# Optimization experiments

Hardware: AMD Instinct MI355X
Metric: run time of the kernel (lower is better)

## Reference

```python
import jax, jax.numpy as jnp
import numpy as np

N = 200_000          # active voxels
CIN, COUT = 64, 128  # in_filters, out_filters
GRID = (32, 480, 480)  # sparse spatial shape (D, H, W)
NEG_SLOPE = 0.01     # nn.LeakyReLU default
EPS = 1e-5           # BatchNorm1d default


def _build_nbrs():
    """Build rulebook-style neighbor tables for the two submanifold kernels.

    Returns nbr31 [9, N] for kernel (3,1,3) and nbr13 [9, N] for kernel (1,3,3).
    Entry == N means 'no active neighbor' (maps to a zero pad row).
    """
    rng = np.random.default_rng(0)
    prod = GRID[0] * GRID[1] * GRID[2]
    lin = rng.choice(prod, size=N, replace=False)
    z, y, x = np.unravel_index(lin, GRID)
    lut = np.full(prod, N, dtype=np.int64)
    lut[lin] = np.arange(N)

    def nbrs(offsets):
        out = np.full((len(offsets), N), N, dtype=np.int32)
        for k, (dz, dy, dx) in enumerate(offsets):
            zz, yy, xx = z + dz, y + dy, x + dx
            valid = ((zz >= 0) & (zz < GRID[0]) & (yy >= 0) & (yy < GRID[1])
                     & (xx >= 0) & (xx < GRID[2]))
            l2 = (zz * GRID[1] + yy) * GRID[2] + xx
            out[k, valid] = lut[l2[valid]].astype(np.int32)
        return out

    off31 = [(dz, 0, dx) for dz in (-1, 0, 1) for dx in (-1, 0, 1)]  # (3,1,3)
    off13 = [(0, dy, dx) for dy in (-1, 0, 1) for dx in (-1, 0, 1)]  # (1,3,3)
    return nbrs(off31), nbrs(off13)


def setup_inputs() -> dict:
    key = jax.random.key(0)
    ks = jax.random.split(key, 5)
    nbr31, nbr13 = _build_nbrs()
    s_in = (2.0 / (9 * CIN)) ** 0.5
    s_out = (2.0 / (9 * COUT)) ** 0.5
    ones = jnp.ones((COUT,), jnp.float32)
    zeros = jnp.zeros((COUT,), jnp.float32)
    return {
        "feats": jax.random.normal(ks[0], (N, CIN), jnp.float32),
        "W1": jax.random.normal(ks[1], (9, CIN, COUT), jnp.float32) * s_in,
        "W1_2": jax.random.normal(ks[2], (9, COUT, COUT), jnp.float32) * s_out,
        "W2": jax.random.normal(ks[3], (9, CIN, COUT), jnp.float32) * s_in,
        "W3": jax.random.normal(ks[4], (9, COUT, COUT), jnp.float32) * s_out,
        "g0": ones, "b0": zeros,      # bn0  (init: weight=1, bias=0)
        "g0_2": ones, "b0_2": zeros,  # bn0_2
        "g1": ones, "b1": zeros,      # bn1
        "g2": ones, "b2": zeros,      # bn2
        "nbr31": jnp.asarray(nbr31),
        "nbr13": jnp.asarray(nbr13),
    }


def _subm_conv(f, W, nbr):
    # f [N, Cin], W [9, Cin, Cout], nbr [9, N] -> [N, Cout]
    fp = jnp.concatenate([f, jnp.zeros((1, f.shape[1]), f.dtype)], axis=0)
    g = fp[nbr]  # gather: [9, N, Cin]
    return jnp.einsum("knc,kcd->nd", g, W)


def _lrelu(f):
    return jnp.where(f >= 0, f, NEG_SLOPE * f)


def _bn(f, gamma, beta):
    # BatchNorm1d training-mode batch stats (biased variance) over voxel dim
    m = jnp.mean(f, axis=0)
    v = jnp.mean(jnp.square(f), axis=0) - m * m
    return (f - m) * jax.lax.rsqrt(v + EPS) * gamma + beta


def reference(feats, W1, W1_2, W2, W3, g0, b0, g0_2, b0_2, g1, b1, g2, b2,
              nbr31, nbr13):
    shortcut = _bn(_lrelu(_subm_conv(feats, W1, nbr31)), g0, b0)
    shortcut = _bn(_lrelu(_subm_conv(shortcut, W1_2, nbr13)), g0_2, b0_2)
    resA = _bn(_lrelu(_subm_conv(feats, W2, nbr13)), g1, b1)
    resA = _bn(_lrelu(_subm_conv(resA, W3, nbr31)), g2, b2)
    return resA + shortcut
```

## Files before the change

### kernel.cpp

```cpp
#include <hip/hip_runtime.h>

#define NV 200000
#define NCH 391
#define PCAP 56
#define CG 3125
#define PN 3516
#define RB1 110

typedef __attribute__((ext_vector_type(8))) short sh8;
typedef __attribute__((ext_vector_type(4))) float f32x4;
typedef __attribute__((ext_vector_type(2))) unsigned int u32x2;

__device__ inline unsigned short f2bf(float f) {
  unsigned int u = __builtin_bit_cast(unsigned int, f);
  u += 0x7FFFu + ((u >> 16) & 1u);
  return (unsigned short)(u >> 16);
}
__device__ inline float bf2f(unsigned short h) {
  unsigned int u = ((unsigned int)h) << 16;
  return __builtin_bit_cast(float, u);
}
__device__ inline float lrelu(float v) { return v >= 0.f ? v : 0.01f * v; }

__global__ __launch_bounds__(256) void prep_k(
    const float* __restrict__ W1, const float* __restrict__ W12,
    const float* __restrict__ W2, const float* __restrict__ W3,
    unsigned short* __restrict__ T1, unsigned short* __restrict__ T12,
    unsigned short* __restrict__ T2, unsigned short* __restrict__ T3,
    const int* __restrict__ nbr31, const int* __restrict__ nbr13,
    int2* __restrict__ pairs, int* __restrict__ cc) {
  __shared__ unsigned short lt[64 * 130];
  __shared__ int base_s[4];
  __shared__ int run;
  int bx = blockIdx.x;
  const int tid = threadIdx.x;
  if (bx < 36) {
    const float* src;
    unsigned short* dst;
    int cin, k;
    if (bx < 9) { src = W1; dst = T1; cin = 64; k = bx; }
    else if (bx < 18) { src = W2; dst = T2; cin = 64; k = bx - 9; }
    else if (bx < 27) { src = W12; dst = T12; cin = 128; k = bx - 18; }
    else { src = W3; dst = T3; cin = 128; k = bx - 27; }
    src += (size_t)k * cin * 128;
    dst += (size_t)k * 128 * cin;
    const int cmask = cin - 1;
    const int csh = (cin == 64) ? 6 : 7;
    for (int h = 0; h < 2; ++h) {
      if (h) __syncthreads();
      const int tot = cin * 64;
      for (int e = tid; e < tot; e += 256) {
        const int c = e >> 6, dd = e & 63;
        lt[dd * 130 + c] = f2bf(src[c * 128 + h * 64 + dd]);
      }
      __syncthreads();
      for (int o = tid; o < tot; o += 256) {
        const int dl = o >> csh, c = o & cmask;
        dst[(size_t)(h * 64 + dl) * cin + c] = lt[dl * 130 + c];
      }
    }
    return;
  }
  bx -= 36;
  const int slot = bx / NCH, chunk = bx % NCH;
  const int table = slot >> 3, kk = slot & 7;
  const int k = kk + (kk >= 4);
  const int* nb = (table ? nbr13 : nbr31) + (size_t)k * NV;
  const int lane = tid & 63, wv = tid >> 6;
  if (tid == 0) run = 0;
  __syncthreads();
  int2* pw = pairs + (size_t)(slot * NCH + chunk) * PCAP;
#pragma unroll
  for (int i = 0; i < 2; ++i) {
    const int n = chunk * 512 + i * 256 + tid;
    const int val = (n < NV) ? nb[n] : NV;
    const bool valid = (val != NV);
    const unsigned long long m = __ballot(valid);
    const int loff = __popcll(m & ((1ull << lane) - 1ull));
    if (lane == 0) base_s[wv] = __popcll(m);
    __syncthreads();
    int wbase = run;
    for (int w = 0; w < wv; ++w) wbase += base_s[w];
    if (valid) {
      const int pos = wbase + loff;
      if (pos < PCAP) {
        int2 pr;
        pr.x = val;
        pr.y = n;
        pw[pos] = pr;
      }
    }
    __syncthreads();
    if (tid == 0) run += base_s[0] + base_s[1] + base_s[2] + base_s[3];
    __syncthreads();
  }
  if (tid == 0) cc[slot * NCH + chunk] = min(run, PCAP);
}

#define STATS_EMIT(ACC, PART, PROW)                                             \
  {                                                                             \
    f32x4 ssum[2], ssq[2];                                                      \
    _Pragma("unroll") for (int mt = 0; mt < 2; ++mt) {                          \
      ssum[mt] = (f32x4){0.f, 0.f, 0.f, 0.f};                                   \
      ssq[mt] = (f32x4){0.f, 0.f, 0.f, 0.f};                                    \
      _Pragma("unroll") for (int nt = 0; nt < 4; ++nt)                          \
          _Pragma("unroll") for (int q = 0; q < 4; ++q) {                       \
        const float f = lrelu(ACC[mt][nt][q]);                                  \
        ssum[mt][q] += f;                                                       \
        ssq[mt][q] += f * f;                                                    \
      }                                                                         \
      _Pragma("unroll") for (int off = 1; off < 16; off <<= 1)                  \
          _Pragma("unroll") for (int q = 0; q < 4; ++q) {                       \
        ssum[mt][q] += __shfl_xor(ssum[mt][q], off);                            \
        ssq[mt][q] += __shfl_xor(ssq[mt][q], off);                              \
      }                                                                         \
      if (l15 == 0) {                                                           \
        const int d0 = (wv * 2 + mt) * 16 + l4 * 4;                             \
        *(f32x4*)(PART + (size_t)(PROW)*256 + d0) = ssum[mt];                   \
        *(f32x4*)(PART + (size_t)(PROW)*256 + 128 + d0) = ssq[mt];              \
      }                                                                         \
    }                                                                           \
  }

#define TILE_OUT(ACC, YPTR)                                                     \
  {                                                                             \
    __syncthreads();                                                            \
    _Pragma("unroll") for (int mt = 0; mt < 2; ++mt)                            \
        _Pragma("unroll") for (int nt = 0; nt < 4; ++nt) {                      \
      u32x2 pk;                                                                 \
      pk[0] = (unsigned)f2bf(ACC[mt][nt][0]) |                                  \
              ((unsigned)f2bf(ACC[mt][nt][1]) << 16);                           \
      pk[1] = (unsigned)f2bf(ACC[mt][nt][2]) |                                  \
              ((unsigned)f2bf(ACC[mt][nt][3]) << 16);                           \
      *(u32x2*)(&lds[(nt * 16 + l15) * 136 + (wv * 2 + mt) * 16 + l4 * 4]) = pk;\
    }                                                                           \
    __syncthreads();                                                            \
    _Pragma("unroll") for (int j = 0; j < 4; ++j) {                             \
      const int row = j * 16 + (tid >> 4);                                      \
      const int c16 = tid & 15;                                                 \
      const sh8 v = *(const sh8*)(&lds[row * 136 + c16 * 8]);                   \
      *(sh8*)(YPTR + (size_t)(row0 + row) * 128 + c16 * 8) = v;                 \
    }                                                                           \
  }

__global__ __launch_bounds__(256) void center2_k(
    const float* __restrict__ X, const unsigned short* __restrict__ W1t,
    const unsigned short* __restrict__ W2t, unsigned short* __restrict__ Y1,
    unsigned short* __restrict__ Y2, float* __restrict__ PA,
    float* __restrict__ PB) {
  constexpr int CIN = 64, CH = 8;
  __shared__ unsigned short lds[64 * 136];
  const int tid = threadIdx.x, lane = tid & 63, wv = tid >> 6;
  const int l15 = lane & 15, l4 = lane >> 4;
  const int prow = blockIdx.x;
  const int row0 = prow * 64;
  const int js = tid & 7;
#pragma unroll
  for (int i = 0; i < 2; ++i) {
    const int r = (i * 256 + tid) >> 3;
    const f32x4 a = *(const f32x4*)(X + (size_t)(row0 + r) * CIN + js * 8);
    const f32x4 b = *(const f32x4*)(X + (size_t)(row0 + r) * CIN + js * 8 + 4);
    sh8 o;
#pragma unroll
    for (int j = 0; j < 4; ++j) {
      o[j] = (short)f2bf(a[j]);
      o[4 + j] = (short)f2bf(b[j]);
    }
    *(sh8*)(lds + ((size_t)r * CH + (js ^ (r & 7))) * 8) = o;
  }
  __syncthreads();

  f32x4 acc1[2][4], acc2[2][4];
#pragma unroll
  for (int mt = 0; mt < 2; ++mt)
#pragma unroll
    for (int nt = 0; nt < 4; ++nt) {
      acc1[mt][nt] = (f32x4){0.f, 0.f, 0.f, 0.f};
      acc2[mt][nt] = (f32x4){0.f, 0.f, 0.f, 0.f};
    }
  const unsigned short* W1K = W1t + (size_t)(4 * 128) * CIN;
  const unsigned short* W2K = W2t + (size_t)(4 * 128) * CIN;
#pragma unroll
  for (int s = 0; s < 2; ++s) {
    sh8 aw1[2], aw2[2];
#pragma unroll
    for (int mt = 0; mt < 2; ++mt) {
      const int d = (wv * 2 + mt) * 16 + l15;
      aw1[mt] = *(const sh8*)(W1K + (size_t)d * CIN + s * 32 + l4 * 8);
      aw2[mt] = *(const sh8*)(W2K + (size_t)d * CIN + s * 32 + l4 * 8);
    }
#pragma unroll
    for (int nt = 0; nt < 4; ++nt) {
      const int r = nt * 16 + l15;
      const int j = s * 4 + l4;
      const sh8 bx = *(const sh8*)(lds + ((size_t)r * CH + (j ^ (r & 7))) * 8);
#pragma unroll
      for (int mt = 0; mt < 2; ++mt) {
        acc1[mt][nt] =
            __builtin_amdgcn_mfma_f32_16x16x32_bf16(aw1[mt], bx, acc1[mt][nt], 0, 0, 0);
        acc2[mt][nt] =
            __builtin_amdgcn_mfma_f32_16x16x32_bf16(aw2[mt], bx, acc2[mt][nt], 0, 0, 0);
      }
    }
  }
  STATS_EMIT(acc1, PA, prow)
  STATS_EMIT(acc2, PB, prow)
  TILE_OUT(acc1, Y1)
  __syncthreads();
  TILE_OUT(acc2, Y2)
}

__global__ __launch_bounds__(256) void c128m_k(
    const unsigned short* __restrict__ y1, const unsigned short* __restrict__ y2,
    const unsigned short* __restrict__ T12, const unsigned short* __restrict__ T3,
    const float* __restrict__ ab, unsigned short* __restrict__ ysc,
    unsigned short* __restrict__ y3, float* __restrict__ PA,
    float* __restrict__ PB) {
  constexpr int CIN = 128, CH = 16;
  __shared__ unsigned short lds[64 * 136];
  const int bx = blockIdx.x;
  const bool first = bx < CG;
  const unsigned short* X = first ? y1 : y2;
  const unsigned short* Wt = first ? T12 : T3;
  const float* abp = first ? ab : ab + 256;
  unsigned short* Y = first ? ysc : y3;
  float* PART = first ? PA : PB;
  const int prow = first ? bx : bx - CG;
  const int row0 = prow * 64;
  const int tid = threadIdx.x, lane = tid & 63, wv = tid >> 6;
  const int l15 = lane & 15, l4 = lane >> 4;
  const int js = tid & 15;
  const f32x4 aL = *(const f32x4*)(abp + js * 8);
  const f32x4 aH = *(const f32x4*)(abp + js * 8 + 4);
  const f32x4 bL = *(const f32x4*)(abp + 128 + js * 8);
  const f32x4 bH = *(const f32x4*)(abp + 128 + js * 8 + 4);
#pragma unroll
  for (int i = 0; i < 4; ++i) {
    const int r = (i * 256 + tid) >> 4;
    const sh8 v = *(const sh8*)(X + (size_t)(row0 + r) * CIN + js * 8);
    sh8 o;
#pragma unroll
    for (int j = 0; j < 4; ++j) {
      o[j] = (short)f2bf(lrelu(bf2f((unsigned short)v[j])) * aL[j] + bL[j]);
      o[4 + j] = (short)f2bf(lrelu(bf2f((unsigned short)v[4 + j])) * aH[j] + bH[j]);
    }
    *(sh8*)(lds + ((size_t)r * CH + (js ^ (r & 7))) * 8) = o;
  }
  __syncthreads();

  f32x4 acc[2][4];
#pragma unroll
  for (int mt = 0; mt < 2; ++mt)
#pragma unroll
    for (int nt = 0; nt < 4; ++nt) acc[mt][nt] = (f32x4){0.f, 0.f, 0.f, 0.f};

  const unsigned short* WtK = Wt + (size_t)(4 * 128) * CIN;
#pragma unroll
  for (int s = 0; s < 4; ++s) {
    sh8 aw[2];
#pragma unroll
    for (int mt = 0; mt < 2; ++mt) {
      const int d = (wv * 2 + mt) * 16 + l15;
      aw[mt] = *(const sh8*)(WtK + (size_t)d * CIN + s * 32 + l4 * 8);
    }
#pragma unroll
    for (int nt = 0; nt < 4; ++nt) {
      const int r = nt * 16 + l15;
      const int j = s * 4 + l4;
      const sh8 bxv = *(const sh8*)(lds + ((size_t)r * CH + (j ^ (r & 7))) * 8);
#pragma unroll
      for (int mt = 0; mt < 2; ++mt)
        acc[mt][nt] =
            __builtin_amdgcn_mfma_f32_16x16x32_bf16(aw[mt], bxv, acc[mt][nt], 0, 0, 0);
    }
  }
  STATS_EMIT(acc, PART, prow)
  TILE_OUT(acc, Y)
}

__global__ __launch_bounds__(256) void off64_k(
    const float* __restrict__ X, const unsigned short* __restrict__ T1,
    const unsigned short* __restrict__ T2, const int2* __restrict__ pairs,
    const int* __restrict__ cc, unsigned short* __restrict__ y1,
    unsigned short* __restrict__ y2, float* __restrict__ PA,
    float* __restrict__ PB) {
  constexpr int CIN = 64, CH = 8;
  const int layer = blockIdx.x / NCH, chunk = blockIdx.x % NCH;
  const unsigned short* Wt = layer ? T2 : T1;
  unsigned short* Y = layer ? y2 : y1;
  float* PD = layer ? PB : PA;
  const int* ccl = cc + layer * 8 * NCH;
  const int2* pl = pairs + (size_t)layer * 8 * NCH * PCAP;
  __shared__ unsigned short tile[64 * CIN];
  const int tid = threadIdx.x, lane = tid & 63, wv = tid >> 6;
  const int l15 = lane & 15, l4 = lane >> 4;
  const int js = tid & 7;
  f32x4 ds[2], dq[2];
#pragma unroll
  for (int mt = 0; mt < 2; ++mt) {
    ds[mt] = (f32x4){0.f, 0.f, 0.f, 0.f};
    dq[mt] = (f32x4){0.f, 0.f, 0.f, 0.f};
  }

  for (int kk = 0; kk < 8; ++kk) {
    const int n0 = ccl[kk * NCH + chunk];
    if (n0 == 0) continue;
    const int k = kk + (kk >= 4);
    const unsigned short* WtK = Wt + (size_t)k * 128 * CIN;
    const int2* pw = pl + (size_t)(kk * NCH + chunk) * PCAP;
    __syncthreads();
#pragma unroll
    for (int i = 0; i < 2; ++i) {
      const int r = (i * 256 + tid) >> 3;
      const int in = (r < n0) ? pw[r].x : NV;
      sh8 o = (sh8){0, 0, 0, 0, 0, 0, 0, 0};
      if (in != NV) {
        const f32x4 a = *(const f32x4*)(X + (size_t)in * CIN + js * 8);
        const f32x4 b = *(const f32x4*)(X + (size_t)in * CIN + js * 8 + 4);
#pragma unroll
        for (int j = 0; j < 4; ++j) {
          o[j] = (short)f2bf(a[j]);
          o[4 + j] = (short)f2bf(b[j]);
        }
      }
      *(sh8*)(tile + ((size_t)r * CH + (js ^ (r & 7))) * 8) = o;
    }
    __syncthreads();

    f32x4 acc[2][4];
#pragma unroll
    for (int mt = 0; mt < 2; ++mt)
#pragma unroll
      for (int nt = 0; nt < 4; ++nt) acc[mt][nt] = (f32x4){0.f, 0.f, 0.f, 0.f};
#pragma unroll
    for (int s = 0; s < 2; ++s) {
      sh8 aw[2];
#pragma unroll
      for (int mt = 0; mt < 2; ++mt) {
        const int d = (wv * 2 + mt) * 16 + l15;
        aw[mt] = *(const sh8*)(WtK + (size_t)d * CIN + s * 32 + l4 * 8);
      }
#pragma unroll
      for (int nt = 0; nt < 4; ++nt) {
        const int r = nt * 16 + l15;
        const int j = s * 4 + l4;
        const sh8 bxv = *(const sh8*)(tile + ((size_t)r * CH + (j ^ (r & 7))) * 8);
#pragma unroll
        for (int mt = 0; mt < 2; ++mt)
          acc[mt][nt] =
              __builtin_amdgcn_mfma_f32_16x16x32_bf16(aw[mt], bxv, acc[mt][nt], 0, 0, 0);
      }
    }
#pragma unroll
    for (int mt = 0; mt < 2; ++mt)
#pragma unroll
      for (int nt = 0; nt < 4; ++nt) {
        const int rr = nt * 16 + l15;
        const int out = (rr < n0) ? pw[rr].y : NV;
        if (out == NV) continue;
        const int d0 = (wv * 2 + mt) * 16 + l4 * 4;
        unsigned short* p = Y + (size_t)out * 128 + d0;
        const u32x2 old = *(const u32x2*)p;
        u32x2 nw;
        float of[4], sf[4];
        of[0] = bf2f((unsigned short)(old[0] & 0xffff));
        of[1] = bf2f((unsigned short)(old[0] >> 16));
        of[2] = bf2f((unsigned short)(old[1] & 0xffff));
        of[3] = bf2f((unsigned short)(old[1] >> 16));
#pragma unroll
        for (int q = 0; q < 4; ++q) {
          sf[q] = of[q] + acc[mt][nt][q];
          const float ln = lrelu(sf[q]), lo = lrelu(of[q]);
          ds[mt][q] += ln - lo;
          dq[mt][q] += ln * ln - lo * lo;
        }
        nw[0] = (unsigned)f2bf(sf[0]) | ((unsigned)f2bf(sf[1]) << 16);
        nw[1] = (unsigned)f2bf(sf[2]) | ((unsigned)f2bf(sf[3]) << 16);
        *(u32x2*)p = nw;
      }
  }
#pragma unroll
  for (int mt = 0; mt < 2; ++mt) {
#pragma unroll
    for (int off = 1; off < 16; off <<= 1)
#pragma unroll
      for (int q = 0; q < 4; ++q) {
        ds[mt][q] += __shfl_xor(ds[mt][q], off);
        dq[mt][q] += __shfl_xor(dq[mt][q], off);
      }
    if (l15 == 0) {
      const int d0 = (wv * 2 + mt) * 16 + l4 * 4;
      *(f32x4*)(PD + (size_t)(CG + chunk) * 256 + d0) = ds[mt];
      *(f32x4*)(PD + (size_t)(CG + chunk) * 256 + 128 + d0) = dq[mt];
    }
  }
}

__global__ __launch_bounds__(256) void off128m_k(
    const unsigned short* __restrict__ y1, const unsigned short* __restrict__ y2,
    const unsigned short* __restrict__ T12, const unsigned short* __restrict__ T3,
    const int2* __restrict__ pairs, const int* __restrict__ cc,
    const float* __restrict__ ab, unsigned short* __restrict__ ysc,
    unsigned short* __restrict__ y3, float* __restrict__ PA,
    float* __restrict__ PB) {
  constexpr int CIN = 128, CH = 16;
  const int lay = blockIdx.x / NCH, chunk = blockIdx.x % NCH;
  const unsigned short* X = lay ? y2 : y1;
  const unsigned short* Wt = lay ? T3 : T12;
  const float* abp = lay ? ab + 256 : ab;
  unsigned short* Y = lay ? y3 : ysc;
  float* PD = lay ? PB : PA;
  const int2* pt = pairs + (lay ? 0 : (size_t)8 * NCH * PCAP);
  const int* ct = cc + (lay ? 0 : 8 * NCH);
  __shared__ unsigned short tile[64 * CIN];
  const int tid = threadIdx.x, lane = tid & 63, wv = tid >> 6;
  const int l15 = lane & 15, l4 = lane >> 4;
  const int js = tid & 15;
  const f32x4 aL = *(const f32x4*)(abp + js * 8);
  const f32x4 aH = *(const f32x4*)(abp + js * 8 + 4);
  const f32x4 bL = *(const f32x4*)(abp + 128 + js * 8);
  const f32x4 bH = *(const f32x4*)(abp + 128 + js * 8 + 4);
  f32x4 ds[2], dq[2];
#pragma unroll
  for (int mt = 0; mt < 2; ++mt) {
    ds[mt] = (f32x4){0.f, 0.f, 0.f, 0.f};
    dq[mt] = (f32x4){0.f, 0.f, 0.f, 0.f};
  }

  for (int kk = 0; kk < 8; ++kk) {
    const int n0 = ct[kk * NCH + chunk];
    if (n0 == 0) continue;
    const int k = kk + (kk >= 4);
    const unsigned short* WtK = Wt + (size_t)k * 128 * CIN;
    const int2* pw = pt + (size_t)(kk * NCH + chunk) * PCAP;
    __syncthreads();
#pragma unroll
    for (int i = 0; i < 4; ++i) {
      const int r = (i * 256 + tid) >> 4;
      const int in = (r < n0) ? pw[r].x : NV;
      sh8 o = (sh8){0, 0, 0, 0, 0, 0, 0, 0};
      if (in != NV) {
        const sh8 v = *(const sh8*)(X + (size_t)in * CIN + js * 8);
#pragma unroll
        for (int j = 0; j < 4; ++j) {
          o[j] = (short)f2bf(lrelu(bf2f((unsigned short)v[j])) * aL[j] + bL[j]);
          o[4 + j] = (short)f2bf(lrelu(bf2f((unsigned short)v[4 + j])) * aH[j] + bH[j]);
        }
      }
      *(sh8*)(tile + ((size_t)r * CH + (js ^ (r & 7))) * 8) = o;
    }
    __syncthreads();

    f32x4 acc[2][4];
#pragma unroll
    for (int mt = 0; mt < 2; ++mt)
#pragma unroll
      for (int nt = 0; nt < 4; ++nt) acc[mt][nt] = (f32x4){0.f, 0.f, 0.f, 0.f};
#pragma unroll
    for (int s = 0; s < 4; ++s) {
      sh8 aw[2];
#pragma unroll
      for (int mt = 0; mt < 2; ++mt) {
        const int d = (wv * 2 + mt) * 16 + l15;
        aw[mt] = *(const sh8*)(WtK + (size_t)d * CIN + s * 32 + l4 * 8);
      }
#pragma unroll
      for (int nt = 0; nt < 4; ++nt) {
        const int r = nt * 16 + l15;
        const int j = s * 4 + l4;
        const sh8 bxv = *(const sh8*)(tile + ((size_t)r * CH + (j ^ (r & 7))) * 8);
#pragma unroll
        for (int mt = 0; mt < 2; ++mt)
          acc[mt][nt] =
              __builtin_amdgcn_mfma_f32_16x16x32_bf16(aw[mt], bxv, acc[mt][nt], 0, 0, 0);
      }
    }
#pragma unroll
    for (int mt = 0; mt < 2; ++mt)
#pragma unroll
      for (int nt = 0; nt < 4; ++nt) {
        const int rr = nt * 16 + l15;
        const int out = (rr < n0) ? pw[rr].y : NV;
        if (out == NV) continue;
        const int d0 = (wv * 2 + mt) * 16 + l4 * 4;
        unsigned short* p = Y + (size_t)out * 128 + d0;
        const u32x2 old = *(const u32x2*)p;
        u32x2 nw;
        float of[4], sf[4];
        of[0] = bf2f((unsigned short)(old[0] & 0xffff));
        of[1] = bf2f((unsigned short)(old[0] >> 16));
        of[2] = bf2f((unsigned short)(old[1] & 0xffff));
        of[3] = bf2f((unsigned short)(old[1] >> 16));
#pragma unroll
        for (int q = 0; q < 4; ++q) {
          sf[q] = of[q] + acc[mt][nt][q];
          const float ln = lrelu(sf[q]), lo = lrelu(of[q]);
          ds[mt][q] += ln - lo;
          dq[mt][q] += ln * ln - lo * lo;
        }
        nw[0] = (unsigned)f2bf(sf[0]) | ((unsigned)f2bf(sf[1]) << 16);
        nw[1] = (unsigned)f2bf(sf[2]) | ((unsigned)f2bf(sf[3]) << 16);
        *(u32x2*)p = nw;
      }
  }
#pragma unroll
  for (int mt = 0; mt < 2; ++mt) {
#pragma unroll
    for (int off = 1; off < 16; off <<= 1)
#pragma unroll
      for (int q = 0; q < 4; ++q) {
        ds[mt][q] += __shfl_xor(ds[mt][q], off);
        dq[mt][q] += __shfl_xor(dq[mt][q], off);
      }
    if (l15 == 0) {
      const int d0 = (wv * 2 + mt) * 16 + l4 * 4;
      *(f32x4*)(PD + (size_t)(CG + chunk) * 256 + d0) = ds[mt];
      *(f32x4*)(PD + (size_t)(CG + chunk) * 256 + 128 + d0) = dq[mt];
    }
  }
}

__global__ __launch_bounds__(256) void red1_k(const float* __restrict__ PA,
                                              const float* __restrict__ PB,
                                              float* __restrict__ RA,
                                              float* __restrict__ RB) {
  const int tb = blockIdx.x / RB1;
  const int b = blockIdx.x % RB1;
  const float* P = tb ? PB : PA;
  float* R = tb ? RB : RA;
  const int c = threadIdx.x;
  const int r0 = b * 32;
  const int r1 = (r0 + 32 < PN) ? r0 + 32 : PN;
  float s = 0.f;
#pragma unroll 4
  for (int r = r0; r < r1; ++r) s += P[(size_t)r * 256 + c];
  R[(size_t)b * 256 + c] = s;
}

__global__ __launch_bounds__(1024) void fin2_k(
    const float* __restrict__ RA, const float* __restrict__ gA,
    const float* __restrict__ btA, float* __restrict__ abA,
    const float* __restrict__ RB, const float* __restrict__ gB,
    const float* __restrict__ btB, float* __restrict__ abB) {
  const float* R = blockIdx.x ? RB : RA;
  const float* g = blockIdx.x ? gB : gA;
  const float* bt = blockIdx.x ? btB : btA;
  float* abo = blockIdx.x ? abB : abA;
  __shared__ float S[1024];
  const int t = threadIdx.x;
  const int c = t & 255, grp = t >> 8;
  float s = 0.f;
  for (int b = grp; b < RB1; b += 4) s += R[(size_t)b * 256 + c];
  S[t] = s;
  __syncthreads();
  if (t < 256) S[t] = S[t] + S[256 + t] + S[512 + t] + S[768 + t];
  __syncthreads();
  if (t < 128) {
    const float m = S[t] * (1.0f / (float)NV);
    const float v = S[128 + t] * (1.0f / (float)NV) - m * m;
    const float a = g[t] * rsqrtf(v + 1e-5f);
    abo[t] = a;
    abo[128 + t] = bt[t] - m * a;
  }
}

__global__ __launch_bounds__(256) void final_k(const unsigned short* __restrict__ y3,
                                               const unsigned short* __restrict__ ysc,
                                               const float* __restrict__ ab3,
                                               const float* __restrict__ ab1,
                                               float* __restrict__ out) {
  const long i = (long)blockIdx.x * 256 + threadIdx.x;
  if (i >= (long)NV * 16) return;
  const long base = i * 8;
  const int c0 = (int)(base & 127);
  const sh8 v3 = *(const sh8*)(y3 + base);
  const sh8 vs = *(const sh8*)(ysc + base);
  const f32x4 a3L = *(const f32x4*)(ab3 + c0);
  const f32x4 a3H = *(const f32x4*)(ab3 + c0 + 4);
  const f32x4 b3L = *(const f32x4*)(ab3 + 128 + c0);
  const f32x4 b3H = *(const f32x4*)(ab3 + 128 + c0 + 4);
  const f32x4 a1L = *(const f32x4*)(ab1 + c0);
  const f32x4 a1H = *(const f32x4*)(ab1 + c0 + 4);
  const f32x4 b1L = *(const f32x4*)(ab1 + 128 + c0);
  const f32x4 b1H = *(const f32x4*)(ab1 + 128 + c0 + 4);
  f32x4 oL, oH;
#pragma unroll
  for (int j = 0; j < 4; ++j) {
    oL[j] = a3L[j] * lrelu(bf2f((unsigned short)v3[j])) + b3L[j] +
            a1L[j] * lrelu(bf2f((unsigned short)vs[j])) + b1L[j];
    oH[j] = a3H[j] * lrelu(bf2f((unsigned short)v3[4 + j])) + b3H[j] +
            a1H[j] * lrelu(bf2f((unsigned short)vs[4 + j])) + b1H[j];
  }
  *(f32x4*)(out + base) = oL;
  *(f32x4*)(out + base + 4) = oH;
}

extern "C" void kernel_launch(void* const* d_in, const int* in_sizes, int n_in,
                              void* d_out, int out_size, void* d_ws, size_t ws_size,
                              hipStream_t stream) {
  const float* feats = (const float*)d_in[0];
  const float* W1 = (const float*)d_in[1];
  const float* W12 = (const float*)d_in[2];
  const float* W2 = (const float*)d_in[3];
  const float* W3 = (const float*)d_in[4];
  const float* g0 = (const float*)d_in[5];
  const float* b0 = (const float*)d_in[6];
  const float* g02 = (const float*)d_in[7];
  const float* b02 = (const float*)d_in[8];
  const float* g1 = (const float*)d_in[9];
  const float* b1 = (const float*)d_in[10];
  const float* g2 = (const float*)d_in[11];
  const float* b2 = (const float*)d_in[12];
  const int* nbr31 = (const int*)d_in[13];
  const int* nbr13 = (const int*)d_in[14];
  float* out = (float*)d_out;

  char* ws = (char*)d_ws;
  size_t off = 0;
  auto alloc = [&](size_t bytes) {
    char* p = ws + off;
    off = (off + bytes + 255) & ~(size_t)255;
    return p;
  };

  unsigned short* T1 = (unsigned short*)alloc((size_t)9 * 128 * 64 * 2);
  unsigned short* T2 = (unsigned short*)alloc((size_t)9 * 128 * 64 * 2);
  unsigned short* T12 = (unsigned short*)alloc((size_t)9 * 128 * 128 * 2);
  unsigned short* T3 = (unsigned short*)alloc((size_t)9 * 128 * 128 * 2);
  unsigned short* y1 = (unsigned short*)alloc((size_t)NV * 128 * 2);
  unsigned short* y2 = (unsigned short*)alloc((size_t)NV * 128 * 2);
  unsigned short* ysc = (unsigned short*)alloc((size_t)NV * 128 * 2);
  unsigned short* y3 = (unsigned short*)alloc((size_t)NV * 128 * 2);
  float* PA = (float*)alloc((size_t)PN * 256 * 4);
  float* PB = (float*)alloc((size_t)PN * 256 * 4);
  float* RA = (float*)alloc((size_t)RB1 * 256 * 4);
  float* RB = (float*)alloc((size_t)RB1 * 256 * 4);
  float* ab = (float*)alloc(1024 * 4);
  int* cc = (int*)alloc((size_t)16 * NCH * 4);
  int2* pairs = (int2*)alloc((size_t)16 * NCH * PCAP * 8);


  prep_k<<<36 + 16 * NCH, 256, 0, stream>>>(W1, W12, W2, W3, T1, T12, T2, T3,
                                            nbr31, nbr13, pairs, cc);
  center2_k<<<CG, 256, 0, stream>>>(feats, T1, T2, y1, y2, PA, PB);
  off64_k<<<2 * NCH, 256, 0, stream>>>(feats, T1, T2, pairs, cc, y1, y2, PA, PB);
  red1_k<<<2 * RB1, 256, 0, stream>>>(PA, PB, RA, RB);
  fin2_k<<<2, 1024, 0, stream>>>(RA, g0, b0, ab + 0, RB, g1, b1, ab + 256);
  c128m_k<<<2 * CG, 256, 0, stream>>>(y1, y2, T12, T3, ab, ysc, y3, PA, PB);
  off128m_k<<<2 * NCH, 256, 0, stream>>>(y1, y2, T12, T3, pairs, cc, ab, ysc, y3,
                                         PA, PB);
  red1_k<<<2 * RB1, 256, 0, stream>>>(PA, PB, RA, RB);
  fin2_k<<<2, 1024, 0, stream>>>(RA, g02, b02, ab + 512, RB, g2, b2, ab + 768);
  final_k<<<12500, 256, 0, stream>>>(y3, ysc, ab + 768, ab + 512, out);
}
```

Baseline: 288.0 us.

## Replace compacted pair lists with output-stationary per-tile neighbour gather convolution

Drops the prep-time compaction of neighbour pairs and the separate offset kernels, which did scattered bf16 read-modify-write updates to the outputs. Each 64-row output tile now loops over all nine kernel offsets. For each offset it gathers neighbour rows directly from the nbr tables into LDS and accumulates with MFMA in registers. A block-wide OR skips an offset only when the tile has no valid neighbour at all. This removes kernel launches, the pair buffers and the scatter RMW traffic, but runs much more MFMA work on mostly zero rows and adds a barrier per offset.

```diff
diff --git a/kernel.cpp b/kernel.cpp
--- a/kernel.cpp
+++ b/kernel.cpp
@@ -1,11 +1,9 @@
 #include <hip/hip_runtime.h>
 
 #define NV 200000
-#define NCH 391
-#define PCAP 56
 #define CG 3125
-#define PN 3516
-#define RB1 110
+#define PN 3125
+#define RB1 98
 
 typedef __attribute__((ext_vector_type(8))) short sh8;
 typedef __attribute__((ext_vector_type(4))) float f32x4;
@@ -26,75 +24,34 @@
     const float* __restrict__ W1, const float* __restrict__ W12,
     const float* __restrict__ W2, const float* __restrict__ W3,
     unsigned short* __restrict__ T1, unsigned short* __restrict__ T12,
-    unsigned short* __restrict__ T2, unsigned short* __restrict__ T3,
-    const int* __restrict__ nbr31, const int* __restrict__ nbr13,
-    int2* __restrict__ pairs, int* __restrict__ cc) {
+    unsigned short* __restrict__ T2, unsigned short* __restrict__ T3) {
   __shared__ unsigned short lt[64 * 130];
-  __shared__ int base_s[4];
-  __shared__ int run;
-  int bx = blockIdx.x;
+  const int bx = blockIdx.x;
   const int tid = threadIdx.x;
-  if (bx < 36) {
-    const float* src;
-    unsigned short* dst;
-    int cin, k;
-    if (bx < 9) { src = W1; dst = T1; cin = 64; k = bx; }
-    else if (bx < 18) { src = W2; dst = T2; cin = 64; k = bx - 9; }
-    else if (bx < 27) { src = W12; dst = T12; cin = 128; k = bx - 18; }
-    else { src = W3; dst = T3; cin = 128; k = bx - 27; }
-    src += (size_t)k * cin * 128;
-    dst += (size_t)k * 128 * cin;
-    const int cmask = cin - 1;
-    const int csh = (cin == 64) ? 6 : 7;
-    for (int h = 0; h < 2; ++h) {
-      if (h) __syncthreads();
-      const int tot = cin * 64;
-      for (int e = tid; e < tot; e += 256) {
-        const int c = e >> 6, dd = e & 63;
-        lt[dd * 130 + c] = f2bf(src[c * 128 + h * 64 + dd]);
-      }
-      __syncthreads();
-      for (int o = tid; o < tot; o += 256) {
-        const int dl = o >> csh, c = o & cmask;
-        dst[(size_t)(h * 64 + dl) * cin + c] = lt[dl * 130 + c];
-      }
-    }
-    return;
-  }
-  bx -= 36;
-  const int slot = bx / NCH, chunk = bx % NCH;
-  const int table = slot >> 3, kk = slot & 7;
-  const int k = kk + (kk >= 4);
-  const int* nb = (table ? nbr13 : nbr31) + (size_t)k * NV;
-  const int lane = tid & 63, wv = tid >> 6;
-  if (tid == 0) run = 0;
-  __syncthreads();
-  int2* pw = pairs + (size_t)(slot * NCH + chunk) * PCAP;
-#pragma unroll
-  for (int i = 0; i < 2; ++i) {
-    const int n = chunk * 512 + i * 256 + tid;
-    const int val = (n < NV) ? nb[n] : NV;
-    const bool valid = (val != NV);
-    const unsigned long long m = __ballot(valid);
-    const int loff = __popcll(m & ((1ull << lane) - 1ull));
-    if (lane == 0) base_s[wv] = __popcll(m);
+  const float* src;
+  unsigned short* dst;
+  int cin, k;
+  if (bx < 9) { src = W1; dst = T1; cin = 64; k = bx; }
+  else if (bx < 18) { src = W2; dst = T2; cin = 64; k = bx - 9; }
+  else if (bx < 27) { src = W12; dst = T12; cin = 128; k = bx - 18; }
+  else { src = W3; dst = T3; cin = 128; k = bx - 27; }
+  src += (size_t)k * cin * 128;
+  dst += (size_t)k * 128 * cin;
+  const int cmask = cin - 1;
+  const int csh = (cin == 64) ? 6 : 7;
+  for (int h = 0; h < 2; ++h) {
+    if (h) __syncthreads();
+    const int tot = cin * 64;
+    for (int e = tid; e < tot; e += 256) {
+      const int c = e >> 6, dd = e & 63;
+      lt[dd * 130 + c] = f2bf(src[c * 128 + h * 64 + dd]);
+    }
     __syncthreads();
-    int wbase = run;
-    for (int w = 0; w < wv; ++w) wbase += base_s[w];
-    if (valid) {
-      const int pos = wbase + loff;
-      if (pos < PCAP) {
-        int2 pr;
-        pr.x = val;
-        pr.y = n;
-        pw[pos] = pr;
-      }
-    }
-    __syncthreads();
-    if (tid == 0) run += base_s[0] + base_s[1] + base_s[2] + base_s[3];
-    __syncthreads();
-  }
-  if (tid == 0) cc[slot * NCH + chunk] = min(run, PCAP);
+    for (int o = tid; o < tot; o += 256) {
+      const int dl = o >> csh, c = o & cmask;
+      dst[(size_t)(h * 64 + dl) * cin + c] = lt[dl * 130 + c];
+    }
+  }
 }
 
 #define STATS_EMIT(ACC, PART, PROW)                                             \
@@ -143,9 +100,10 @@
     }                                                                           \
   }
 
-__global__ __launch_bounds__(256) void center2_k(
-    const float* __restrict__ X, const unsigned short* __restrict__ W1t,
-    const unsigned short* __restrict__ W2t, unsigned short* __restrict__ Y1,
+__global__ __launch_bounds__(256) void conv64_k(
+    const float* __restrict__ X, const unsigned short* __restrict__ T1,
+    const unsigned short* __restrict__ T2, const int* __restrict__ nbr31,
+    const int* __restrict__ nbr13, unsigned short* __restrict__ Y1,
     unsigned short* __restrict__ Y2, float* __restrict__ PA,
     float* __restrict__ PB) {
   constexpr int CIN = 64, CH = 8;
@@ -155,6 +113,38 @@
   const int prow = blockIdx.x;
   const int row0 = prow * 64;
   const int js = tid & 7;
+
+  f32x4 acc1[2][4], acc2[2][4];
+#pragma unroll
+  for (int mt = 0; mt < 2; ++mt)
+#pragma unroll
+    for (int nt = 0; nt < 4; ++nt) {
+      acc1[mt][nt] = (f32x4){0.f, 0.f, 0.f, 0.f};
+      acc2[mt][nt] = (f32x4){0.f, 0.f, 0.f, 0.f};
+    }
+
+  auto domfma = [&](const unsigned short* WtK, f32x4(&acc)[2][4]) {
+#pragma unroll
+    for (int s = 0; s < 2; ++s) {
+      sh8 aw[2];
+#pragma unroll
+      for (int mt = 0; mt < 2; ++mt) {
+        const int d = (wv * 2 + mt) * 16 + l15;
+        aw[mt] = *(const sh8*)(WtK + (size_t)d * CIN + s * 32 + l4 * 8);
+      }
+#pragma unroll
+      for (int nt = 0; nt < 4; ++nt) {
+        const int r = nt * 16 + l15;
+        const int j = s * 4 + l4;
+        const sh8 bxv = *(const sh8*)(lds + ((size_t)r * CH + (j ^ (r & 7))) * 8);
+#pragma unroll
+        for (int mt = 0; mt < 2; ++mt)
+          acc[mt][nt] =
+              __builtin_amdgcn_mfma_f32_16x16x32_bf16(aw[mt], bxv, acc[mt][nt], 0, 0, 0);
+      }
+    }
+  };
+
 #pragma unroll
   for (int i = 0; i < 2; ++i) {
     const int r = (i * 256 + tid) >> 3;
@@ -169,50 +159,50 @@
     *(sh8*)(lds + ((size_t)r * CH + (js ^ (r & 7))) * 8) = o;
   }
   __syncthreads();
-
-  f32x4 acc1[2][4], acc2[2][4];
-#pragma unroll
-  for (int mt = 0; mt < 2; ++mt)
-#pragma unroll
-    for (int nt = 0; nt < 4; ++nt) {
-      acc1[mt][nt] = (f32x4){0.f, 0.f, 0.f, 0.f};
-      acc2[mt][nt] = (f32x4){0.f, 0.f, 0.f, 0.f};
-    }
-  const unsigned short* W1K = W1t + (size_t)(4 * 128) * CIN;
-  const unsigned short* W2K = W2t + (size_t)(4 * 128) * CIN;
-#pragma unroll
-  for (int s = 0; s < 2; ++s) {
-    sh8 aw1[2], aw2[2];
-#pragma unroll
-    for (int mt = 0; mt < 2; ++mt) {
-      const int d = (wv * 2 + mt) * 16 + l15;
-      aw1[mt] = *(const sh8*)(W1K + (size_t)d * CIN + s * 32 + l4 * 8);
-      aw2[mt] = *(const sh8*)(W2K + (size_t)d * CIN + s * 32 + l4 * 8);
-    }
-#pragma unroll
-    for (int nt = 0; nt < 4; ++nt) {
-      const int r = nt * 16 + l15;
-      const int j = s * 4 + l4;
-      const sh8 bx = *(const sh8*)(lds + ((size_t)r * CH + (j ^ (r & 7))) * 8);
-#pragma unroll
-      for (int mt = 0; mt < 2; ++mt) {
-        acc1[mt][nt] =
-            __builtin_amdgcn_mfma_f32_16x16x32_bf16(aw1[mt], bx, acc1[mt][nt], 0, 0, 0);
-        acc2[mt][nt] =
-            __builtin_amdgcn_mfma_f32_16x16x32_bf16(aw2[mt], bx, acc2[mt][nt], 0, 0, 0);
+  domfma(T1 + (size_t)(4 * 128) * CIN, acc1);
+  domfma(T2 + (size_t)(4 * 128) * CIN, acc2);
+  __syncthreads();
+
+  for (int t = 0; t < 16; ++t) {
+    const int kk = t & 7;
+    const int k = kk + (kk >= 4);
+    const int* nb = ((t < 8) ? nbr31 : nbr13) + (size_t)k * NV;
+    int vflag = 0;
+#pragma unroll
+    for (int i = 0; i < 2; ++i) {
+      const int r = (i * 256 + tid) >> 3;
+      const int in = nb[row0 + r];
+      sh8 o = (sh8){0, 0, 0, 0, 0, 0, 0, 0};
+      if (in != NV) {
+        vflag = 1;
+        const f32x4 a = *(const f32x4*)(X + (size_t)in * CIN + js * 8);
+        const f32x4 b = *(const f32x4*)(X + (size_t)in * CIN + js * 8 + 4);
+#pragma unroll
+        for (int j = 0; j < 4; ++j) {
+          o[j] = (short)f2bf(a[j]);
+          o[4 + j] = (short)f2bf(b[j]);
+        }
       }
-    }
-  }
+      *(sh8*)(lds + ((size_t)r * CH + (js ^ (r & 7))) * 8) = o;
+    }
+    const int any = __syncthreads_or(vflag);
+    if (any) {
+      if (t < 8) domfma(T1 + (size_t)k * 128 * CIN, acc1);
+      else domfma(T2 + (size_t)k * 128 * CIN, acc2);
+      __syncthreads();
+    }
+  }
+
   STATS_EMIT(acc1, PA, prow)
   STATS_EMIT(acc2, PB, prow)
   TILE_OUT(acc1, Y1)
-  __syncthreads();
   TILE_OUT(acc2, Y2)
 }
 
-__global__ __launch_bounds__(256) void c128m_k(
+__global__ __launch_bounds__(256) void conv128_k(
     const unsigned short* __restrict__ y1, const unsigned short* __restrict__ y2,
     const unsigned short* __restrict__ T12, const unsigned short* __restrict__ T3,
+    const int* __restrict__ nbr31, const int* __restrict__ nbr13,
     const float* __restrict__ ab, unsigned short* __restrict__ ysc,
     unsigned short* __restrict__ y3, float* __restrict__ PA,
     float* __restrict__ PB) {
@@ -222,6 +212,7 @@
   const bool first = bx < CG;
   const unsigned short* X = first ? y1 : y2;
   const unsigned short* Wt = first ? T12 : T3;
+  const int* nbt = first ? nbr13 : nbr31;
   const float* abp = first ? ab : ab + 256;
   unsigned short* Y = first ? ysc : y3;
   float* PART = first ? PA : PB;
@@ -234,19 +225,6 @@
   const f32x4 aH = *(const f32x4*)(abp + js * 8 + 4);
   const f32x4 bL = *(const f32x4*)(abp + 128 + js * 8);
   const f32x4 bH = *(const f32x4*)(abp + 128 + js * 8 + 4);
-#pragma unroll
-  for (int i = 0; i < 4; ++i) {
-    const int r = (i * 256 + tid) >> 4;
-    const sh8 v = *(const sh8*)(X + (size_t)(row0 + r) * CIN + js * 8);
-    sh8 o;
-#pragma unroll
-    for (int j = 0; j < 4; ++j) {
-      o[j] = (short)f2bf(lrelu(bf2f((unsigned short)v[j])) * aL[j] + bL[j]);
-      o[4 + j] = (short)f2bf(lrelu(bf2f((unsigned short)v[4 + j])) * aH[j] + bH[j]);
-    }
-    *(sh8*)(lds + ((size_t)r * CH + (js ^ (r & 7))) * 8) = o;
-  }
-  __syncthreads();
 
   f32x4 acc[2][4];
 #pragma unroll
@@ -254,192 +232,16 @@
 #pragma unroll
     for (int nt = 0; nt < 4; ++nt) acc[mt][nt] = (f32x4){0.f, 0.f, 0.f, 0.f};
 
-  const unsigned short* WtK = Wt + (size_t)(4 * 128) * CIN;
-#pragma unroll
-  for (int s = 0; s < 4; ++s) {
-    sh8 aw[2];
-#pragma unroll
-    for (int mt = 0; mt < 2; ++mt) {
-      const int d = (wv * 2 + mt) * 16 + l15;
-      aw[mt] = *(const sh8*)(WtK + (size_t)d * CIN + s * 32 + l4 * 8);
-    }
-#pragma unroll
-    for (int nt = 0; nt < 4; ++nt) {
-      const int r = nt * 16 + l15;
-      const int j = s * 4 + l4;
-      const sh8 bxv = *(const sh8*)(lds + ((size_t)r * CH + (j ^ (r & 7))) * 8);
-#pragma unroll
-      for (int mt = 0; mt < 2; ++mt)
-        acc[mt][nt] =
-            __builtin_amdgcn_mfma_f32_16x16x32_bf16(aw[mt], bxv, acc[mt][nt], 0, 0, 0);
-    }
-  }
-  STATS_EMIT(acc, PART, prow)
-  TILE_OUT(acc, Y)
-}
-
-__global__ __launch_bounds__(256) void off64_k(
-    const float* __restrict__ X, const unsigned short* __restrict__ T1,
-    const unsigned short* __restrict__ T2, const int2* __restrict__ pairs,
-    const int* __restrict__ cc, unsigned short* __restrict__ y1,
-    unsigned short* __restrict__ y2, float* __restrict__ PA,
-    float* __restrict__ PB) {
-  constexpr int CIN = 64, CH = 8;
-  const int layer = blockIdx.x / NCH, chunk = blockIdx.x % NCH;
-  const unsigned short* Wt = layer ? T2 : T1;
-  unsigned short* Y = layer ? y2 : y1;
-  float* PD = layer ? PB : PA;
-  const int* ccl = cc + layer * 8 * NCH;
-  const int2* pl = pairs + (size_t)layer * 8 * NCH * PCAP;
-  __shared__ unsigned short tile[64 * CIN];
-  const int tid = threadIdx.x, lane = tid & 63, wv = tid >> 6;
-  const int l15 = lane & 15, l4 = lane >> 4;
-  const int js = tid & 7;
-  f32x4 ds[2], dq[2];
-#pragma unroll
-  for (int mt = 0; mt < 2; ++mt) {
-    ds[mt] = (f32x4){0.f, 0.f, 0.f, 0.f};
-    dq[mt] = (f32x4){0.f, 0.f, 0.f, 0.f};
-  }
-
-  for (int kk = 0; kk < 8; ++kk) {
-    const int n0 = ccl[kk * NCH + chunk];
-    if (n0 == 0) continue;
-    const int k = kk + (kk >= 4);
-    const unsigned short* WtK = Wt + (size_t)k * 128 * CIN;
-    const int2* pw = pl + (size_t)(kk * NCH + chunk) * PCAP;
-    __syncthreads();
-#pragma unroll
-    for (int i = 0; i < 2; ++i) {
-      const int r = (i * 256 + tid) >> 3;
-      const int in = (r < n0) ? pw[r].x : NV;
+  for (int k = 0; k < 9; ++k) {
+    const int* nb = nbt + (size_t)k * NV;
+    int vflag = 0;
+#pragma unroll
+    for (int i = 0; i < 4; ++i) {
+      const int r = (i * 256 + tid) >> 4;
+      const int in = nb[row0 + r];
       sh8 o = (sh8){0, 0, 0, 0, 0, 0, 0, 0};
       if (in != NV) {
-        const f32x4 a = *(const f32x4*)(X + (size_t)in * CIN + js * 8);
-        const f32x4 b = *(const f32x4*)(X + (size_t)in * CIN + js * 8 + 4);
-#pragma unroll
-        for (int j = 0; j < 4; ++j) {
-          o[j] = (short)f2bf(a[j]);
-          o[4 + j] = (short)f2bf(b[j]);
-        }
-      }
-      *(sh8*)(tile + ((size_t)r * CH + (js ^ (r & 7))) * 8) = o;
-    }
-    __syncthreads();
-
-    f32x4 acc[2][4];
-#pragma unroll
-    for (int mt = 0; mt < 2; ++mt)
-#pragma unroll
-      for (int nt = 0; nt < 4; ++nt) acc[mt][nt] = (f32x4){0.f, 0.f, 0.f, 0.f};
-#pragma unroll
-    for (int s = 0; s < 2; ++s) {
-      sh8 aw[2];
-#pragma unroll
-      for (int mt = 0; mt < 2; ++mt) {
-        const int d = (wv * 2 + mt) * 16 + l15;
-        aw[mt] = *(const sh8*)(WtK + (size_t)d * CIN + s * 32 + l4 * 8);
-      }
-#pragma unroll
-      for (int nt = 0; nt < 4; ++nt) {
-        const int r = nt * 16 + l15;
-        const int j = s * 4 + l4;
-        const sh8 bxv = *(const sh8*)(tile + ((size_t)r * CH + (j ^ (r & 7))) * 8);
-#pragma unroll
-        for (int mt = 0; mt < 2; ++mt)
-          acc[mt][nt] =
-              __builtin_amdgcn_mfma_f32_16x16x32_bf16(aw[mt], bxv, acc[mt][nt], 0, 0, 0);
-      }
-    }
-#pragma unroll
-    for (int mt = 0; mt < 2; ++mt)
-#pragma unroll
-      for (int nt = 0; nt < 4; ++nt) {
-        const int rr = nt * 16 + l15;
-        const int out = (rr < n0) ? pw[rr].y : NV;
-        if (out == NV) continue;
-        const int d0 = (wv * 2 + mt) * 16 + l4 * 4;
-        unsigned short* p = Y + (size_t)out * 128 + d0;
-        const u32x2 old = *(const u32x2*)p;
-        u32x2 nw;
-        float of[4], sf[4];
-        of[0] = bf2f((unsigned short)(old[0] & 0xffff));
-        of[1] = bf2f((unsigned short)(old[0] >> 16));
-        of[2] = bf2f((unsigned short)(old[1] & 0xffff));
-        of[3] = bf2f((unsigned short)(old[1] >> 16));
-#pragma unroll
-        for (int q = 0; q < 4; ++q) {
-          sf[q] = of[q] + acc[mt][nt][q];
-          const float ln = lrelu(sf[q]), lo = lrelu(of[q]);
-          ds[mt][q] += ln - lo;
-          dq[mt][q] += ln * ln - lo * lo;
-        }
-        nw[0] = (unsigned)f2bf(sf[0]) | ((unsigned)f2bf(sf[1]) << 16);
-        nw[1] = (unsigned)f2bf(sf[2]) | ((unsigned)f2bf(sf[3]) << 16);
-        *(u32x2*)p = nw;
-      }
-  }
-#pragma unroll
-  for (int mt = 0; mt < 2; ++mt) {
-#pragma unroll
-    for (int off = 1; off < 16; off <<= 1)
-#pragma unroll
-      for (int q = 0; q < 4; ++q) {
-        ds[mt][q] += __shfl_xor(ds[mt][q], off);
-        dq[mt][q] += __shfl_xor(dq[mt][q], off);
-      }
-    if (l15 == 0) {
-      const int d0 = (wv * 2 + mt) * 16 + l4 * 4;
-      *(f32x4*)(PD + (size_t)(CG + chunk) * 256 + d0) = ds[mt];
-      *(f32x4*)(PD + (size_t)(CG + chunk) * 256 + 128 + d0) = dq[mt];
-    }
-  }
-}
-
-__global__ __launch_bounds__(256) void off128m_k(
-    const unsigned short* __restrict__ y1, const unsigned short* __restrict__ y2,
-    const unsigned short* __restrict__ T12, const unsigned short* __restrict__ T3,
-    const int2* __restrict__ pairs, const int* __restrict__ cc,
-    const float* __restrict__ ab, unsigned short* __restrict__ ysc,
-    unsigned short* __restrict__ y3, float* __restrict__ PA,
-    float* __restrict__ PB) {
-  constexpr int CIN = 128, CH = 16;
-  const int lay = blockIdx.x / NCH, chunk = blockIdx.x % NCH;
-  const unsigned short* X = lay ? y2 : y1;
-  const unsigned short* Wt = lay ? T3 : T12;
-  const float* abp = lay ? ab + 256 : ab;
-  unsigned short* Y = lay ? y3 : ysc;
-  float* PD = lay ? PB : PA;
-  const int2* pt = pairs + (lay ? 0 : (size_t)8 * NCH * PCAP);
-  const int* ct = cc + (lay ? 0 : 8 * NCH);
-  __shared__ unsigned short tile[64 * CIN];
-  const int tid = threadIdx.x, lane = tid & 63, wv = tid >> 6;
-  const int l15 = lane & 15, l4 = lane >> 4;
-  const int js = tid & 15;
-  const f32x4 aL = *(const f32x4*)(abp + js * 8);
-  const f32x4 aH = *(const f32x4*)(abp + js * 8 + 4);
-  const f32x4 bL = *(const f32x4*)(abp + 128 + js * 8);
-  const f32x4 bH = *(const f32x4*)(abp + 128 + js * 8 + 4);
-  f32x4 ds[2], dq[2];
-#pragma unroll
-  for (int mt = 0; mt < 2; ++mt) {
-    ds[mt] = (f32x4){0.f, 0.f, 0.f, 0.f};
-    dq[mt] = (f32x4){0.f, 0.f, 0.f, 0.f};
-  }
-
-  for (int kk = 0; kk < 8; ++kk) {
-    const int n0 = ct[kk * NCH + chunk];
-    if (n0 == 0) continue;
-    const int k = kk + (kk >= 4);
-    const unsigned short* WtK = Wt + (size_t)k * 128 * CIN;
-    const int2* pw = pt + (size_t)(kk * NCH + chunk) * PCAP;
-    __syncthreads();
-#pragma unroll
-    for (int i = 0; i < 4; ++i) {
-      const int r = (i * 256 + tid) >> 4;
-      const int in = (r < n0) ? pw[r].x : NV;
-      sh8 o = (sh8){0, 0, 0, 0, 0, 0, 0, 0};
-      if (in != NV) {
+        vflag = 1;
         const sh8 v = *(const sh8*)(X + (size_t)in * CIN + js * 8);
 #pragma unroll
         for (int j = 0; j < 4; ++j) {
@@ -447,77 +249,36 @@
           o[4 + j] = (short)f2bf(lrelu(bf2f((unsigned short)v[4 + j])) * aH[j] + bH[j]);
         }
       }
-      *(sh8*)(tile + ((size_t)r * CH + (js ^ (r & 7))) * 8) = o;
-    }
-    __syncthreads();
-
-    f32x4 acc[2][4];
-#pragma unroll
-    for (int mt = 0; mt < 2; ++mt)
-#pragma unroll
-      for (int nt = 0; nt < 4; ++nt) acc[mt][nt] = (f32x4){0.f, 0.f, 0.f, 0.f};
-#pragma unroll
-    for (int s = 0; s < 4; ++s) {
-      sh8 aw[2];
-#pragma unroll
-      for (int mt = 0; mt < 2; ++mt) {
-        const int d = (wv * 2 + mt) * 16 + l15;
-        aw[mt] = *(const sh8*)(WtK + (size_t)d * CIN + s * 32 + l4 * 8);
+      *(sh8*)(lds + ((size_t)r * CH + (js ^ (r & 7))) * 8) = o;
+    }
+    const int any = __syncthreads_or(vflag);
+    if (any) {
+      const unsigned short* WtK = Wt + (size_t)k * 128 * CIN;
+#pragma unroll
+      for (int s = 0; s < 4; ++s) {
+        sh8 aw[2];
+#pragma unroll
+        for (int mt = 0; mt < 2; ++mt) {
+          const int d = (wv * 2 + mt) * 16 + l15;
+          aw[mt] = *(const sh8*)(WtK + (size_t)d * CIN + s * 32 + l4 * 8);
+        }
+#pragma unroll
+        for (int nt = 0; nt < 4; ++nt) {
+          const int r = nt * 16 + l15;
+          const int j = s * 4 + l4;
+          const sh8 bxv = *(const sh8*)(lds + ((size_t)r * CH + (j ^ (r & 7))) * 8);
+#pragma unroll
+          for (int mt = 0; mt < 2; ++mt)
+            acc[mt][nt] =
+                __builtin_amdgcn_mfma_f32_16x16x32_bf16(aw[mt], bxv, acc[mt][nt], 0, 0, 0);
+        }
       }
-#pragma unroll
-      for (int nt = 0; nt < 4; ++nt) {
-        const int r = nt * 16 + l15;
-        const int j = s * 4 + l4;
-        const sh8 bxv = *(const sh8*)(tile + ((size_t)r * CH + (j ^ (r & 7))) * 8);
-#pragma unroll
-        for (int mt = 0; mt < 2; ++mt)
-          acc[mt][nt] =
-              __builtin_amdgcn_mfma_f32_16x16x32_bf16(aw[mt], bxv, acc[mt][nt], 0, 0, 0);
-      }
-    }
-#pragma unroll
-    for (int mt = 0; mt < 2; ++mt)
-#pragma unroll
-      for (int nt = 0; nt < 4; ++nt) {
-        const int rr = nt * 16 + l15;
-        const int out = (rr < n0) ? pw[rr].y : NV;
-        if (out == NV) continue;
-        const int d0 = (wv * 2 + mt) * 16 + l4 * 4;
-        unsigned short* p = Y + (size_t)out * 128 + d0;
-        const u32x2 old = *(const u32x2*)p;
-        u32x2 nw;
-        float of[4], sf[4];
-        of[0] = bf2f((unsigned short)(old[0] & 0xffff));
-        of[1] = bf2f((unsigned short)(old[0] >> 16));
-        of[2] = bf2f((unsigned short)(old[1] & 0xffff));
-        of[3] = bf2f((unsigned short)(old[1] >> 16));
-#pragma unroll
-        for (int q = 0; q < 4; ++q) {
-          sf[q] = of[q] + acc[mt][nt][q];
-          const float ln = lrelu(sf[q]), lo = lrelu(of[q]);
-          ds[mt][q] += ln - lo;
-          dq[mt][q] += ln * ln - lo * lo;
-        }
-        nw[0] = (unsigned)f2bf(sf[0]) | ((unsigned)f2bf(sf[1]) << 16);
-        nw[1] = (unsigned)f2bf(sf[2]) | ((unsigned)f2bf(sf[3]) << 16);
-        *(u32x2*)p = nw;
-      }
-  }
-#pragma unroll
-  for (int mt = 0; mt < 2; ++mt) {
-#pragma unroll
-    for (int off = 1; off < 16; off <<= 1)
-#pragma unroll
-      for (int q = 0; q < 4; ++q) {
-        ds[mt][q] += __shfl_xor(ds[mt][q], off);
-        dq[mt][q] += __shfl_xor(dq[mt][q], off);
-      }
-    if (l15 == 0) {
-      const int d0 = (wv * 2 + mt) * 16 + l4 * 4;
-      *(f32x4*)(PD + (size_t)(CG + chunk) * 256 + d0) = ds[mt];
-      *(f32x4*)(PD + (size_t)(CG + chunk) * 256 + 128 + d0) = dq[mt];
-    }
-  }
+      __syncthreads();
+    }
+  }
+
+  STATS_EMIT(acc, PART, prow)
+  TILE_OUT(acc, Y)
 }
 
 __global__ __launch_bounds__(256) void red1_k(const float* __restrict__ PA,
@@ -636,19 +397,14 @@
   float* RA = (float*)alloc((size_t)RB1 * 256 * 4);
   float* RB = (float*)alloc((size_t)RB1 * 256 * 4);
   float* ab = (float*)alloc(1024 * 4);
-  int* cc = (int*)alloc((size_t)16 * NCH * 4);
-  int2* pairs = (int2*)alloc((size_t)16 * NCH * PCAP * 8);
-
-
-  prep_k<<<36 + 16 * NCH, 256, 0, stream>>>(W1, W12, W2, W3, T1, T12, T2, T3,
-                                            nbr31, nbr13, pairs, cc);
-  center2_k<<<CG, 256, 0, stream>>>(feats, T1, T2, y1, y2, PA, PB);
-  off64_k<<<2 * NCH, 256, 0, stream>>>(feats, T1, T2, pairs, cc, y1, y2, PA, PB);
+
+
+  prep_k<<<36, 256, 0, stream>>>(W1, W12, W2, W3, T1, T12, T2, T3);
+  conv64_k<<<CG, 256, 0, stream>>>(feats, T1, T2, nbr31, nbr13, y1, y2, PA, PB);
   red1_k<<<2 * RB1, 256, 0, stream>>>(PA, PB, RA, RB);
   fin2_k<<<2, 1024, 0, stream>>>(RA, g0, b0, ab + 0, RB, g1, b1, ab + 256);
-  c128m_k<<<2 * CG, 256, 0, stream>>>(y1, y2, T12, T3, ab, ysc, y3, PA, PB);
-  off128m_k<<<2 * NCH, 256, 0, stream>>>(y1, y2, T12, T3, pairs, cc, ab, ysc, y3,
-                                         PA, PB);
+  conv128_k<<<2 * CG, 256, 0, stream>>>(y1, y2, T12, T3, nbr31, nbr13, ab, ysc,
+                                        y3, PA, PB);
   red1_k<<<2 * RB1, 256, 0, stream>>>(PA, PB, RA, RB);
   fin2_k<<<2, 1024, 0, stream>>>(RA, g02, b02, ab + 512, RB, g2, b2, ab + 768);
   final_k<<<12500, 256, 0, stream>>>(y3, ysc, ab + 768, ab + 512, out);
```

New measurement: 582.2 us. 2.02x slower.
